# Kernel optimization log

Measured on AMD Instinct MI355X. Metric: run time of the kernel, lower is better.

The kernel has to match this reference:

```python
import jax, jax.numpy as jnp
import numpy as np

BS, C, D, HW = 2, 64, 64, 96
HID = 4          # hidden_rnn
R = 16           # SE reduction


def _lstm_layer(x, w_ih, w_hh, b_ih, b_hh):
    # x: [B, T, In] -> outputs [B, T, H]; PyTorch gate order (i, f, g, o)
    b = b_ih + b_hh
    Hd = w_hh.shape[1]
    B = x.shape[0]

    def step(carry, xt):
        h, c = carry
        g = xt @ w_ih.T + h @ w_hh.T + b          # [B, 4H]
        i, f, gg, o = jnp.split(g, 4, axis=-1)
        c = jax.nn.sigmoid(f) * c + jax.nn.sigmoid(i) * jnp.tanh(gg)
        h = jax.nn.sigmoid(o) * jnp.tanh(c)
        return (h, c), h

    h0 = jnp.zeros((B, Hd), x.dtype)
    (_, _), ys = jax.lax.scan(step, (h0, h0), jnp.swapaxes(x, 0, 1))
    return jnp.swapaxes(ys, 0, 1)


def _bilstm(x, layers):
    # layers: list of (wih_f, whh_f, bih_f, bhh_f, wih_b, whh_b, bih_b, bhh_b)
    y = x
    for (wif, whf, bif, bhf, wib, whb, bib, bhb) in layers:
        fwd = _lstm_layer(y, wif, whf, bif, bhf)
        bwd = _lstm_layer(y[:, ::-1], wib, whb, bib, bhb)[:, ::-1]
        y = jnp.concatenate([fwd, bwd], axis=-1)
    return y


def setup_inputs() -> dict:
    key = jax.random.key(0)
    ks = iter(jax.random.split(key, 32))
    k = 1.0 / np.sqrt(HID)
    u = lambda shp: jax.random.uniform(next(ks), shp, jnp.float32, -k, k)

    inp = {"x": jax.random.normal(next(ks), (BS, C, D, HW, HW), jnp.float32)}
    # layer 0 input size 1, layer 1 input size 2*HID
    for li, isz in ((0, 1), (1, 2 * HID)):
        for dr in ("f", "b"):
            inp[f"wih{li}{dr}"] = u((4 * HID, isz))
            inp[f"whh{li}{dr}"] = u((4 * HID, HID))
            inp[f"bih{li}{dr}"] = u((4 * HID,))
            inp[f"bhh{li}{dr}"] = u((4 * HID,))
    feat = 2 * HID * C          # 512
    inp["w1"] = jax.random.normal(next(ks), (feat // R, feat), jnp.float32) / np.sqrt(feat)
    inp["w2"] = jax.random.normal(next(ks), (C, feat // R), jnp.float32) / np.sqrt(feat // R)
    return inp


def reference(x, wih0f, whh0f, bih0f, bhh0f, wih0b, whh0b, bih0b, bhh0b,
              wih1f, whh1f, bih1f, bhh1f, wih1b, whh1b, bih1b, bhh1b, w1, w2):
    bs, c, d = x.shape[:3]
    # squeeze: adaptive avg pool over H, W -> [bs*c, d, 1]
    y = x.mean(axis=(3, 4)).reshape(bs * c, d, 1)
    layers = [(wih0f, whh0f, bih0f, bhh0f, wih0b, whh0b, bih0b, bhh0b),
              (wih1f, whh1f, bih1f, bhh1f, wih1b, whh1b, bih1b, bhh1b)]
    y = _bilstm(y, layers)                 # [bs*c, d, 2*HID]
    y = y[:, -1, :].reshape(bs, -1)        # [bs, 2*HID*c]
    y = jax.nn.sigmoid(jax.nn.relu(y @ w1.T) @ w2.T)   # [bs, c]
    return x * y[:, :, None, None, None]
```

## Files before the change

### kernel.cpp

```cpp
#include <hip/hip_runtime.h>
#include <hip/hip_bf16.h>

#define NSEQ   128
#define SEQLEN 64
#define HWHW   9216
#define CHELEM 589824
#define NCHUNK 144

typedef float v4f __attribute__((ext_vector_type(4)));

__device__ __forceinline__ float sigm(float x) {
    return 1.0f / (1.0f + __expf(-x));
}
__device__ __forceinline__ float tanhfast(float x) {
    x = fmaxf(x, -44.0f);
    float e = __expf(-2.0f * x);
    return (1.0f - e) / (1.0f + e);
}

__global__ __launch_bounds__(256) void mean_kernel(const float* __restrict__ x,
                                                   float* __restrict__ means) {
    const int bidx = blockIdx.x;
    const v4f* xp = (const v4f*)(x + (size_t)bidx * HWHW);
    const int tid = threadIdx.x;
    float sum = 0.f;
#pragma unroll
    for (int i = 0; i < 9; ++i) {
        v4f v = xp[tid + i * 256];
        sum += v[0] + v[1] + v[2] + v[3];
    }
#pragma unroll
    for (int off = 32; off; off >>= 1) sum += __shfl_down(sum, off, 64);
    __shared__ float wsum[4];
    const int wave = tid >> 6, lane = tid & 63;
    if (lane == 0) wsum[wave] = sum;
    __syncthreads();
    if (tid == 0)
        means[bidx] = (wsum[0] + wsum[1] + wsum[2] + wsum[3]) * (1.0f / 9216.0f);
}

__global__ __launch_bounds__(256) void lstm_fc_kernel(
    const float* __restrict__ means,
    const float* __restrict__ wih0f, const float* __restrict__ whh0f,
    const float* __restrict__ bih0f, const float* __restrict__ bhh0f,
    const float* __restrict__ wih0b, const float* __restrict__ whh0b,
    const float* __restrict__ bih0b, const float* __restrict__ bhh0b,
    const float* __restrict__ wih1f, const float* __restrict__ whh1f,
    const float* __restrict__ bih1f, const float* __restrict__ bhh1f,
    const float* __restrict__ wih1b, const float* __restrict__ whh1b,
    const float* __restrict__ bih1b, const float* __restrict__ bhh1b,
    const float* __restrict__ w1,    const float* __restrict__ w2,
    float* __restrict__ l0out,
    float* __restrict__ scl)
{
    const int tid  = threadIdx.x;
    const int s    = tid >> 1;
    const int half = tid & 1;

    __shared__ float lastout[NSEQ][8];
    __shared__ float hidden[64];

    {
        const float* wih = half ? wih0b : wih0f;
        const float* whh = half ? whh0b : whh0f;
        const float* bi  = half ? bih0b : bih0f;
        const float* bh  = half ? bhh0b : bhh0f;
        float Wx[16], B[16], Wh[16][4];
#pragma unroll
        for (int g = 0; g < 16; ++g) {
            Wx[g] = wih[g];
            B[g]  = bi[g] + bh[g];
#pragma unroll
            for (int j = 0; j < 4; ++j) Wh[g][j] = whh[g * 4 + j];
        }
        float h[4] = {0, 0, 0, 0}, c[4] = {0, 0, 0, 0};
        const float* seq = means + s * SEQLEN;
        float xnext = seq[half ? (SEQLEN - 1) : 0];
        for (int t = 0; t < SEQLEN; ++t) {
            const int tt = half ? (SEQLEN - 1 - t) : t;
            const float xt = xnext;
            if (t < SEQLEN - 1) xnext = seq[half ? (SEQLEN - 2 - t) : (t + 1)];
            float g[16];
#pragma unroll
            for (int gi = 0; gi < 16; ++gi)
                g[gi] = fmaf(Wx[gi], xt, B[gi]) + Wh[gi][0] * h[0] + Wh[gi][1] * h[1]
                      + Wh[gi][2] * h[2] + Wh[gi][3] * h[3];
#pragma unroll
            for (int j = 0; j < 4; ++j) {
                c[j] = sigm(g[4 + j]) * c[j] + sigm(g[j]) * tanhfast(g[8 + j]);
                h[j] = sigm(g[12 + j]) * tanhfast(c[j]);
            }
            *(float4*)(l0out + (s * SEQLEN + tt) * 8 + half * 4) =
                make_float4(h[0], h[1], h[2], h[3]);
        }
    }
    __threadfence_block();
    __syncthreads();

    {
        const float* wihr = wih1f + half * 8 * 8;
        const float* whhr = whh1f + half * 8 * 4;
        const float* bir  = bih1f + half * 8;
        const float* bhr  = bhh1f + half * 8;
        float Wx[8][8], Wh[8][4], B[8];
#pragma unroll
        for (int g = 0; g < 8; ++g) {
            B[g] = bir[g] + bhr[g];
#pragma unroll
            for (int k = 0; k < 8; ++k) Wx[g][k] = wihr[g * 8 + k];
#pragma unroll
            for (int j = 0; j < 4; ++j) Wh[g][j] = whhr[g * 4 + j];
        }
        float h[4] = {0, 0, 0, 0}, c[4] = {0, 0, 0, 0};
        const float* base = l0out + s * SEQLEN * 8;
        float4 inA = *(const float4*)(base);
        float4 inB = *(const float4*)(base + 4);
        for (int t = 0; t < SEQLEN; ++t) {
            const float in[8] = {inA.x, inA.y, inA.z, inA.w, inB.x, inB.y, inB.z, inB.w};
            if (t < SEQLEN - 1) {
                inA = *(const float4*)(base + (t + 1) * 8);
                inB = *(const float4*)(base + (t + 1) * 8 + 4);
            }
            float g[8];
#pragma unroll
            for (int gi = 0; gi < 8; ++gi) {
                float acc = B[gi];
#pragma unroll
                for (int k = 0; k < 8; ++k) acc = fmaf(Wx[gi][k], in[k], acc);
#pragma unroll
                for (int j = 0; j < 4; ++j) acc = fmaf(Wh[gi][j], h[j], acc);
                g[gi] = acc;
            }
            float a[4], bg[4];
#pragma unroll
            for (int j = 0; j < 4; ++j) {
                a[j]  = half ? tanhfast(g[j]) : sigm(g[j]);
                bg[j] = sigm(g[4 + j]);
            }
#pragma unroll
            for (int j = 0; j < 4; ++j) {
                const float ax = __shfl_xor(a[j], 1);
                const float bx = __shfl_xor(bg[j], 1);
                const float si = half ? ax    : a[j];
                const float sf = half ? bx    : bg[j];
                const float tg = half ? a[j]  : ax;
                const float so = half ? bg[j] : bx;
                c[j] = fmaf(sf, c[j], si * tg);
                h[j] = so * tanhfast(c[j]);
            }
        }
        if (!half) {
            lastout[s][0] = h[0]; lastout[s][1] = h[1];
            lastout[s][2] = h[2]; lastout[s][3] = h[3];
        }
    }

    {
        const float* wihr = wih1b + half * 8 * 8;
        const float* bir  = bih1b + half * 8;
        const float* bhr  = bhh1b + half * 8;
        const float* base = l0out + (s * SEQLEN + SEQLEN - 1) * 8;
        float4 inA = *(const float4*)(base);
        float4 inB = *(const float4*)(base + 4);
        const float in[8] = {inA.x, inA.y, inA.z, inA.w, inB.x, inB.y, inB.z, inB.w};
        float g[8];
#pragma unroll
        for (int gi = 0; gi < 8; ++gi) {
            float acc = bir[gi] + bhr[gi];
#pragma unroll
            for (int k = 0; k < 8; ++k) acc = fmaf(wihr[gi * 8 + k], in[k], acc);
            g[gi] = acc;
        }
        float a[4], bg[4];
#pragma unroll
        for (int j = 0; j < 4; ++j) {
            a[j]  = half ? tanhfast(g[j]) : sigm(g[j]);
            bg[j] = sigm(g[4 + j]);
        }
#pragma unroll
        for (int j = 0; j < 4; ++j) {
            const float ax = __shfl_xor(a[j], 1);
            const float bx = __shfl_xor(bg[j], 1);
            const float si = half ? ax    : a[j];
            const float tg = half ? a[j]  : ax;
            const float so = half ? bg[j] : bx;
            const float cnew = si * tg;
            const float hnew = so * tanhfast(cnew);
            if (!half) lastout[s][4 + j] = hnew;
        }
    }
    __syncthreads();

    {
        const float* lastflat = &lastout[0][0];
        const int wave = tid >> 6, lane = tid & 63;
#pragma unroll
        for (int r = 0; r < 16; ++r) {
            const int o = wave * 16 + r;
            const int b = o >> 5, m = o & 31;
            float p = 0.f;
#pragma unroll
            for (int i = 0; i < 8; ++i) {
                const int k = lane + i * 64;
                p = fmaf(lastflat[b * 512 + k], w1[m * 512 + k], p);
            }
#pragma unroll
            for (int off = 32; off; off >>= 1) p += __shfl_down(p, off, 64);
            if (lane == 0) hidden[b * 32 + m] = fmaxf(p, 0.f);
        }
    }
    __syncthreads();

    if (tid < 128) {
        const int b = tid >> 6, cc = tid & 63;
        float p = 0.f;
#pragma unroll
        for (int m = 0; m < 32; ++m)
            p = fmaf(hidden[b * 32 + m], w2[cc * 32 + m], p);
        scl[tid] = sigm(p);
    }
}

__global__ __launch_bounds__(256) void scale_kernel(const float* __restrict__ x,
                                                    const float* __restrict__ scl,
                                                    float* __restrict__ out) {
    const int ch    = 127 - blockIdx.y;
    const int chunk = (NCHUNK - 1) - blockIdx.x;
    const float sv = scl[ch];
    const size_t base = (size_t)ch * CHELEM + (size_t)chunk * 4096;
    const v4f* xp = (const v4f*)(x + base);
    v4f* op = (v4f*)(out + base);
    const int tid = threadIdx.x;
#pragma unroll
    for (int i = 0; i < 4; ++i) {
        v4f v = xp[tid + i * 256];
        v *= sv;
        __builtin_nontemporal_store(v, op + tid + i * 256);
    }
}

extern "C" void kernel_launch(void* const* d_in, const int* in_sizes, int n_in,
                              void* d_out, int out_size, void* d_ws, size_t ws_size,
                              hipStream_t stream) {
    const float* x     = (const float*)d_in[0];
    const float* wih0f = (const float*)d_in[1];
    const float* whh0f = (const float*)d_in[2];
    const float* bih0f = (const float*)d_in[3];
    const float* bhh0f = (const float*)d_in[4];
    const float* wih0b = (const float*)d_in[5];
    const float* whh0b = (const float*)d_in[6];
    const float* bih0b = (const float*)d_in[7];
    const float* bhh0b = (const float*)d_in[8];
    const float* wih1f = (const float*)d_in[9];
    const float* whh1f = (const float*)d_in[10];
    const float* bih1f = (const float*)d_in[11];
    const float* bhh1f = (const float*)d_in[12];
    const float* wih1b = (const float*)d_in[13];
    const float* whh1b = (const float*)d_in[14];
    const float* bih1b = (const float*)d_in[15];
    const float* bhh1b = (const float*)d_in[16];
    const float* w1    = (const float*)d_in[17];
    const float* w2    = (const float*)d_in[18];
    float* out = (float*)d_out;

    float* ws    = (float*)d_ws;
    float* means = ws;
    float* l0out = ws + 8192;
    float* scl   = ws + 8192 + 65536;

    mean_kernel<<<dim3(8192), dim3(256), 0, stream>>>(x, means);
    lstm_fc_kernel<<<dim3(1), dim3(256), 0, stream>>>(
        means,
        wih0f, whh0f, bih0f, bhh0f, wih0b, whh0b, bih0b, bhh0b,
        wih1f, whh1f, bih1f, bhh1f, wih1b, whh1b, bih1b, bhh1b,
        w1, w2, l0out, scl);
    scale_kernel<<<dim3(NCHUNK, 128), dim3(256), 0, stream>>>(x, scl, out);
}
```

Baseline: 684.3 us.

## Stage an fp16 copy of x in the mean pass and scale from it

The mean kernel now loads x with nontemporal loads and also writes an fp16 copy of x into the workspace. The scale kernel reads that half-precision copy instead of re-reading x in fp32, and it walks channels and chunks in forward order instead of reverse. The aim is to halve the bytes read in the second pass over the tensor, but the extra fp16 write adds about the same traffic back. Rounding x to fp16 also loses precision in the output, and dropping the reversed traversal gives up reuse of the recently-read tail of x from cache. A redundant threadfence before a syncthreads is removed as well.

```diff
diff --git a/kernel.cpp b/kernel.cpp
--- a/kernel.cpp
+++ b/kernel.cpp
@@ -1,5 +1,6 @@
 #include <hip/hip_runtime.h>
 #include <hip/hip_bf16.h>
+#include <hip/hip_fp16.h>
 
 #define NSEQ   128
 #define SEQLEN 64
@@ -7,7 +8,9 @@
 #define CHELEM 589824
 #define NCHUNK 144
 
-typedef float v4f __attribute__((ext_vector_type(4)));
+typedef float    v4f __attribute__((ext_vector_type(4)));
+typedef _Float16 h4  __attribute__((ext_vector_type(4)));
+typedef _Float16 h8  __attribute__((ext_vector_type(8)));
 
 __device__ __forceinline__ float sigm(float x) {
     return 1.0f / (1.0f + __expf(-x));
@@ -19,15 +22,18 @@
 }
 
 __global__ __launch_bounds__(256) void mean_kernel(const float* __restrict__ x,
-                                                   float* __restrict__ means) {
+                                                   float* __restrict__ means,
+                                                   _Float16* __restrict__ xcopy) {
     const int bidx = blockIdx.x;
     const v4f* xp = (const v4f*)(x + (size_t)bidx * HWHW);
+    h4* cp = (h4*)(xcopy + (size_t)bidx * HWHW);
     const int tid = threadIdx.x;
     float sum = 0.f;
 #pragma unroll
     for (int i = 0; i < 9; ++i) {
-        v4f v = xp[tid + i * 256];
+        v4f v = __builtin_nontemporal_load(xp + tid + i * 256);
         sum += v[0] + v[1] + v[2] + v[3];
+        cp[tid + i * 256] = __builtin_convertvector(v, h4);
     }
 #pragma unroll
     for (int off = 32; off; off >>= 1) sum += __shfl_down(sum, off, 64);
@@ -94,7 +100,6 @@
                 make_float4(h[0], h[1], h[2], h[3]);
         }
     }
-    __threadfence_block();
     __syncthreads();
 
     {
@@ -221,21 +226,25 @@
     }
 }
 
-__global__ __launch_bounds__(256) void scale_kernel(const float* __restrict__ x,
+__global__ __launch_bounds__(256) void scale_kernel(const _Float16* __restrict__ xcopy,
                                                     const float* __restrict__ scl,
                                                     float* __restrict__ out) {
-    const int ch    = 127 - blockIdx.y;
-    const int chunk = (NCHUNK - 1) - blockIdx.x;
+    const int ch    = blockIdx.y;
+    const int chunk = blockIdx.x;
     const float sv = scl[ch];
     const size_t base = (size_t)ch * CHELEM + (size_t)chunk * 4096;
-    const v4f* xp = (const v4f*)(x + base);
+    const h8* cp = (const h8*)(xcopy + base);
     v4f* op = (v4f*)(out + base);
     const int tid = threadIdx.x;
 #pragma unroll
-    for (int i = 0; i < 4; ++i) {
-        v4f v = xp[tid + i * 256];
-        v *= sv;
-        __builtin_nontemporal_store(v, op + tid + i * 256);
+    for (int i = 0; i < 2; ++i) {
+        const int idx = tid + i * 256;
+        h8 hv = cp[idx];
+        v4f lo, hi;
+#pragma unroll
+        for (int j = 0; j < 4; ++j) { lo[j] = (float)hv[j] * sv; hi[j] = (float)hv[4 + j] * sv; }
+        __builtin_nontemporal_store(lo, op + idx * 2);
+        __builtin_nontemporal_store(hi, op + idx * 2 + 1);
     }
 }
 
@@ -267,12 +276,13 @@
     float* means = ws;
     float* l0out = ws + 8192;
     float* scl   = ws + 8192 + 65536;
-
-    mean_kernel<<<dim3(8192), dim3(256), 0, stream>>>(x, means);
+    _Float16* xcopy = (_Float16*)(ws + 8192 + 65536 + 128);
+
+    mean_kernel<<<dim3(8192), dim3(256), 0, stream>>>(x, means, xcopy);
     lstm_fc_kernel<<<dim3(1), dim3(256), 0, stream>>>(
         means,
         wih0f, whh0f, bih0f, bhh0f, wih0b, whh0b, bih0b, bhh0b,
         wih1f, whh1f, bih1f, bhh1f, wih1b, whh1b, bih1b, bhh1b,
         w1, w2, l0out, scl);
-    scale_kernel<<<dim3(NCHUNK, 128), dim3(256), 0, stream>>>(x, scl, out);
-}
+    scale_kernel<<<dim3(NCHUNK, 128), dim3(256), 0, stream>>>(xcopy, scl, out);
+}
```

Result: slower. 706.3 us (+3.2%).
